# Performance work log

Measured on AMD Instinct MI355X. Metric: run time of the kernel, lower is better.

## Reference

```python
import jax, jax.numpy as jnp
import numpy as np

N = 27            # hardcoded node count in the module
D = 1024          # state_dim
E = D * 5         # MHA embed dim = 5120
H = 4             # n_heads


def setup_inputs() -> dict:
    key = jax.random.key(0)
    ks = jax.random.split(key, 6)
    s = 0.02
    return {
        "node_states": jax.random.normal(ks[0], (N, D, 5), jnp.float32),
        "hist_prev": jax.random.normal(ks[1], (N, D, 5), jnp.float32),
        "granger_w": jax.random.normal(ks[2], (1, 2 * E), jnp.float32) * s,
        "granger_b": jnp.zeros((1,), jnp.float32),
        "in_proj_w": jax.random.normal(ks[3], (3 * E, E), jnp.float32) * s,
        "in_proj_b": jnp.zeros((3 * E,), jnp.float32),
        "out_proj_w": jax.random.normal(ks[4], (E, E), jnp.float32) * s,
        "out_proj_b": jnp.zeros((E,), jnp.float32),
        "light_hertz": 500,
    }


def _mha(x, in_w, in_b, out_w, out_b):
    # x: [N, E]; torch MultiheadAttention with q=k=v=x, batch of 1
    qkv = x @ in_w.T + in_b                       # [N, 3E]
    q, k, v = jnp.split(qkv, 3, axis=-1)          # each [N, E]
    hd = E // H
    q = q.reshape(N, H, hd).transpose(1, 0, 2)    # [H, N, hd]
    k = k.reshape(N, H, hd).transpose(1, 0, 2)
    v = v.reshape(N, H, hd).transpose(1, 0, 2)
    scores = jnp.einsum('hqd,hkd->hqk', q, k) / jnp.sqrt(jnp.float32(hd))
    attn = jax.nn.softmax(scores, axis=-1)        # [H, N, N]
    o = jnp.einsum('hqk,hkd->hqd', attn, v)       # [H, N, hd]
    o = o.transpose(1, 0, 2).reshape(N, E)
    return o @ out_w.T + out_b                    # [N, E]


def reference(node_states, hist_prev, granger_w, granger_b,
              in_proj_w, in_proj_b, out_proj_w, out_proj_b, light_hertz):
    node_flat = node_states.reshape(N, E)         # [N, E]
    hist_flat = hist_prev.reshape(N, E)           # [N, E]

    # Granger pairwise test, vectorized: pred_input = [hist[j], node[i]]
    # score[i, j] = sigmoid(hist[j] . w_h + node[i] . w_n + b)
    w_h = granger_w[0, :E]
    w_n = granger_w[0, E:]
    col = node_flat @ w_n                          # [N] -> varies with i
    row = hist_flat @ w_h                          # [N] -> varies with j
    adj = jax.nn.sigmoid(col[:, None] + row[None, :] + granger_b[0])  # [N, N]
    causal_adj = adj * (1.0 - jnp.eye(N, dtype=adj.dtype))            # zero diagonal

    hertz_weight = jnp.clip(jnp.float32(light_hertz) / 1000.0, 0.1, 1.0)
    attended = _mha(node_flat, in_proj_w, in_proj_b, out_proj_w, out_proj_b)
    out = (attended * hertz_weight).reshape(N, D, 5)
    return out, causal_adj
```

## Files before the change

kernel.cpp:

```cpp
#include <hip/hip_runtime.h>

#define NROW 27
#define EDIM 5120
#define QKVDIM 15360
#define HD 1280

typedef __attribute__((ext_vector_type(8))) short bf16x8;
typedef __attribute__((ext_vector_type(4))) float f32x4;

__device__ inline short f2bf(float x) {
    unsigned u = __builtin_bit_cast(unsigned, x);
    u = (u + 0x7FFFu + ((u >> 16) & 1u)) >> 16;
    return (short)u;
}
__device__ inline float bf2f(short h) {
    unsigned u = ((unsigned)(unsigned short)h) << 16;
    return __builtin_bit_cast(float, u);
}

#define KC 64
#define LDK 72

__device__ inline void loadW8(float* wbuf, const float* wp) {
    #pragma unroll
    for (int i = 0; i < 8; ++i)
        *(float4*)&wbuf[4 * i] = ((const float4*)wp)[i];
}
__device__ inline void loadX2(float* xbuf, const float* xp, bool xok) {
    if (xok) {
        *(float4*)&xbuf[0] = ((const float4*)xp)[0];
        *(float4*)&xbuf[4] = ((const float4*)xp)[1];
    } else {
        #pragma unroll
        for (int j = 0; j < 8; ++j) xbuf[j] = 0.f;
    }
}

__global__ __launch_bounds__(256)
void gemm_bf16x2(const float* __restrict__ X, const float* __restrict__ W,
                 float* __restrict__ Cp, int K, int Ntot, int Kblk)
{
    __shared__ short Whi[128][LDK];
    __shared__ short Wlo[128][LDK];
    __shared__ short Xhi[32][LDK];
    __shared__ short Xlo[32][LDK];

    const int tid = threadIdx.x;
    const int n0 = blockIdx.x * 128;
    const int k0 = blockIdx.y * Kblk;

    const int lane = tid & 63;
    const int wv   = tid >> 6;
    const int lm   = lane & 15;
    const int q8   = (lane >> 4) * 8;

    f32x4 acc[2][2] = {};

    const int wr  = tid >> 1;
    const int wkh = (tid & 1) * 32;
    const float* wp = W + (size_t)(n0 + wr) * K + k0 + wkh;
    const int xr = tid >> 3;
    const int xk = (tid & 7) * 8;
    const bool xok = (xr < NROW);
    const float* xp = X + (size_t)(xok ? xr : 0) * K + k0 + xk;

    float wbuf[32], xbuf[8];
    loadW8(wbuf, wp);
    loadX2(xbuf, xp, xok);

    for (int kc = 0; kc < Kblk; kc += KC) {
        #pragma unroll
        for (int g = 0; g < 4; ++g) {
            bf16x8 h8, l8;
            #pragma unroll
            for (int j = 0; j < 8; ++j) {
                float f = wbuf[8 * g + j];
                short h = f2bf(f);
                h8[j] = h;
                l8[j] = f2bf(f - bf2f(h));
            }
            *(bf16x8*)&Whi[wr][wkh + 8 * g] = h8;
            *(bf16x8*)&Wlo[wr][wkh + 8 * g] = l8;
        }
        {
            bf16x8 h8, l8;
            #pragma unroll
            for (int j = 0; j < 8; ++j) {
                short h = f2bf(xbuf[j]);
                h8[j] = h;
                l8[j] = f2bf(xbuf[j] - bf2f(h));
            }
            *(bf16x8*)&Xhi[xr][xk] = h8;
            *(bf16x8*)&Xlo[xr][xk] = l8;
        }
        __syncthreads();

        if (kc + KC < Kblk) {
            wp += KC; xp += KC;
            loadW8(wbuf, wp);
            loadX2(xbuf, xp, xok);
        }

        #pragma unroll
        for (int s = 0; s < 2; ++s) {
            const int ko = 32 * s + q8;
            bf16x8 ah0 = *(const bf16x8*)&Xhi[lm][ko];
            bf16x8 ah1 = *(const bf16x8*)&Xhi[lm + 16][ko];
            bf16x8 al0 = *(const bf16x8*)&Xlo[lm][ko];
            bf16x8 al1 = *(const bf16x8*)&Xlo[lm + 16][ko];
            bf16x8 bh0 = *(const bf16x8*)&Whi[32 * wv + lm][ko];
            bf16x8 bh1 = *(const bf16x8*)&Whi[32 * wv + 16 + lm][ko];
            bf16x8 bl0 = *(const bf16x8*)&Wlo[32 * wv + lm][ko];
            bf16x8 bl1 = *(const bf16x8*)&Wlo[32 * wv + 16 + lm][ko];

            acc[0][0] = __builtin_amdgcn_mfma_f32_16x16x32_bf16(ah0, bh0, acc[0][0], 0, 0, 0);
            acc[0][0] = __builtin_amdgcn_mfma_f32_16x16x32_bf16(ah0, bl0, acc[0][0], 0, 0, 0);
            acc[0][0] = __builtin_amdgcn_mfma_f32_16x16x32_bf16(al0, bh0, acc[0][0], 0, 0, 0);

            acc[0][1] = __builtin_amdgcn_mfma_f32_16x16x32_bf16(ah0, bh1, acc[0][1], 0, 0, 0);
            acc[0][1] = __builtin_amdgcn_mfma_f32_16x16x32_bf16(ah0, bl1, acc[0][1], 0, 0, 0);
            acc[0][1] = __builtin_amdgcn_mfma_f32_16x16x32_bf16(al0, bh1, acc[0][1], 0, 0, 0);

            acc[1][0] = __builtin_amdgcn_mfma_f32_16x16x32_bf16(ah1, bh0, acc[1][0], 0, 0, 0);
            acc[1][0] = __builtin_amdgcn_mfma_f32_16x16x32_bf16(ah1, bl0, acc[1][0], 0, 0, 0);
            acc[1][0] = __builtin_amdgcn_mfma_f32_16x16x32_bf16(al1, bh0, acc[1][0], 0, 0, 0);

            acc[1][1] = __builtin_amdgcn_mfma_f32_16x16x32_bf16(ah1, bh1, acc[1][1], 0, 0, 0);
            acc[1][1] = __builtin_amdgcn_mfma_f32_16x16x32_bf16(ah1, bl1, acc[1][1], 0, 0, 0);
            acc[1][1] = __builtin_amdgcn_mfma_f32_16x16x32_bf16(al1, bh1, acc[1][1], 0, 0, 0);
        }
        __syncthreads();
    }

    const size_t base = (size_t)blockIdx.y * NROW * Ntot;
    #pragma unroll
    for (int mi = 0; mi < 2; ++mi) {
        #pragma unroll
        for (int r = 0; r < 4; ++r) {
            const int m = mi * 16 + (lane >> 4) * 4 + r;
            if (m < NROW) {
                #pragma unroll
                for (int ni = 0; ni < 2; ++ni) {
                    const int n = n0 + 32 * wv + ni * 16 + lm;
                    Cp[base + (size_t)m * Ntot + n] = acc[mi][ni][r];
                }
            }
        }
    }
}

__global__ __launch_bounds__(256)
void reduce_kernel(const float* __restrict__ Cp, const float* __restrict__ bias,
                   float* __restrict__ out, int Ntot, int nky, const int* __restrict__ hz,
                   const float* __restrict__ cr, const float* __restrict__ gb,
                   float* __restrict__ adj)
{
    if (adj && blockIdx.x == gridDim.x - 1) {
        for (int t = threadIdx.x; t < NROW * NROW; t += 256) {
            const int i = t / NROW, j = t % NROW;
            float v = 0.f;
            if (i != j) {
                float z = cr[i] + cr[NROW + j] + gb[0];
                v = 1.0f / (1.0f + expf(-z));
            }
            adj[t] = v;
        }
        return;
    }
    const int idx = blockIdx.x * 256 + threadIdx.x;
    const int total4 = NROW * Ntot / 4;
    if (idx >= total4) return;
    float4 s = ((const float4*)Cp)[idx];
    for (int k = 1; k < nky; ++k) {
        float4 p = ((const float4*)(Cp + (size_t)k * NROW * Ntot))[idx];
        s.x += p.x; s.y += p.y; s.z += p.z; s.w += p.w;
    }
    const int n = (idx * 4) % Ntot;
    float4 b = *(const float4*)(bias + n);
    s.x += b.x; s.y += b.y; s.z += b.z; s.w += b.w;
    if (hz) {
        float h = (float)hz[0] * 0.001f;
        float sc = fminf(fmaxf(h, 0.1f), 1.0f);
        s.x *= sc; s.y *= sc; s.z *= sc; s.w *= sc;
    }
    ((float4*)out)[idx] = s;
}

__global__ __launch_bounds__(256)
void colrow_kernel(const float* __restrict__ node, const float* __restrict__ hist,
                   const float* __restrict__ gw, float* __restrict__ cr)
{
    const int b = blockIdx.x;
    const float* x = (b < NROW) ? node + (size_t)b * EDIM : hist + (size_t)(b - NROW) * EDIM;
    const float* w = (b < NROW) ? gw + EDIM : gw;
    const int tid = threadIdx.x;
    float a = 0.f;
    for (int f = tid; f < EDIM / 4; f += 256) {
        float4 xv = ((const float4*)x)[f];
        float4 wv = ((const float4*)w)[f];
        a += xv.x * wv.x + xv.y * wv.y + xv.z * wv.z + xv.w * wv.w;
    }
    #pragma unroll
    for (int off = 32; off; off >>= 1) a += __shfl_down(a, off);
    __shared__ float red[4];
    if ((tid & 63) == 0) red[tid >> 6] = a;
    __syncthreads();
    if (tid == 0) cr[b] = red[0] + red[1] + red[2] + red[3];
}

__global__ __launch_bounds__(256)
void attn_kernel(const float* __restrict__ qkv, float* __restrict__ O)
{
    __shared__ float qs[HD];
    __shared__ float sc[NROW];
    __shared__ float pr[NROW];
    const int bx = blockIdx.x;
    const int h = bx & 3;
    const int i = bx >> 2;
    const int tid = threadIdx.x;

    const size_t qoff = (size_t)i * QKVDIM + (size_t)h * HD;
    for (int d = tid; d < HD; d += 256) qs[d] = qkv[qoff + d];
    __syncthreads();

    const int wid = tid >> 6, lane = tid & 63;
    for (int j = wid; j < NROW; j += 4) {
        const float* kr = qkv + (size_t)j * QKVDIM + EDIM + (size_t)h * HD;
        float a = 0.f;
        #pragma unroll
        for (int it = 0; it < 5; ++it) {
            int d4 = lane + 64 * it;
            float4 k4 = *(const float4*)(kr + 4 * d4);
            float4 q4 = *(const float4*)(qs + 4 * d4);
            a += q4.x * k4.x + q4.y * k4.y + q4.z * k4.z + q4.w * k4.w;
        }
        #pragma unroll
        for (int off = 32; off; off >>= 1) a += __shfl_down(a, off);
        if (lane == 0) sc[j] = a * 0.02795084971874737f;
    }
    __syncthreads();

    float mxv = -1e30f;
    for (int j = 0; j < NROW; ++j) mxv = fmaxf(mxv, sc[j]);
    float s = 0.f;
    for (int j = 0; j < NROW; ++j) s += expf(sc[j] - mxv);
    if (tid < NROW) pr[tid] = expf(sc[tid] - mxv) / s;
    __syncthreads();

    for (int d4 = tid; d4 < HD / 4; d4 += 256) {
        float4 o = make_float4(0.f, 0.f, 0.f, 0.f);
        for (int j = 0; j < NROW; ++j) {
            const float4 v4 = *(const float4*)(qkv + (size_t)j * QKVDIM + 2 * EDIM + (size_t)h * HD + 4 * d4);
            const float p = pr[j];
            o.x = fmaf(p, v4.x, o.x);
            o.y = fmaf(p, v4.y, o.y);
            o.z = fmaf(p, v4.z, o.z);
            o.w = fmaf(p, v4.w, o.w);
        }
        *(float4*)(O + (size_t)i * EDIM + (size_t)h * HD + 4 * d4) = o;
    }
}

extern "C" void kernel_launch(void* const* d_in, const int* in_sizes, int n_in,
                              void* d_out, int out_size, void* d_ws, size_t ws_size,
                              hipStream_t stream)
{
    const float* node = (const float*)d_in[0];
    const float* hist = (const float*)d_in[1];
    const float* gw   = (const float*)d_in[2];
    const float* gb   = (const float*)d_in[3];
    const float* inw  = (const float*)d_in[4];
    const float* inb  = (const float*)d_in[5];
    const float* outw = (const float*)d_in[6];
    const float* outb = (const float*)d_in[7];
    const int*   hz   = (const int*)d_in[8];

    float* out = (float*)d_out;

    float* Cp1  = (float*)d_ws;
    float* qkvf = Cp1 + (size_t)8 * NROW * QKVDIM;
    float* Obuf = qkvf + (size_t)NROW * QKVDIM;
    float* Cp2  = Obuf + (size_t)NROW * EDIM;
    float* cr   = Cp2 + (size_t)16 * NROW * EDIM;

    colrow_kernel<<<54, 256, 0, stream>>>(node, hist, gw, cr);

    gemm_bf16x2<<<dim3(120, 8), 256, 0, stream>>>(node, inw, Cp1, EDIM, QKVDIM, EDIM / 8);
    reduce_kernel<<<NROW * QKVDIM / 4 / 256, 256, 0, stream>>>(
        Cp1, inb, qkvf, QKVDIM, 8, nullptr, nullptr, nullptr, nullptr);

    attn_kernel<<<108, 256, 0, stream>>>(qkvf, Obuf);

    gemm_bf16x2<<<dim3(40, 16), 256, 0, stream>>>(Obuf, outw, Cp2, EDIM, EDIM, EDIM / 16);
    reduce_kernel<<<NROW * EDIM / 4 / 256 + 1, 256, 0, stream>>>(
        Cp2, outb, out, EDIM, 16, hz, cr, gb, out + (size_t)NROW * EDIM);
}
```

Measured before the change: 542.2 us.

## Load weight MFMA fragments directly into registers, double-buffer X tile in LDS

```diff
diff --git a/kernel.cpp b/kernel.cpp
--- a/kernel.cpp
+++ b/kernel.cpp
@@ -21,11 +21,6 @@
 #define KC 64
 #define LDK 72
 
-__device__ inline void loadW8(float* wbuf, const float* wp) {
-    #pragma unroll
-    for (int i = 0; i < 8; ++i)
-        *(float4*)&wbuf[4 * i] = ((const float4*)wp)[i];
-}
 __device__ inline void loadX2(float* xbuf, const float* xp, bool xok) {
     if (xok) {
         *(float4*)&xbuf[0] = ((const float4*)xp)[0];
@@ -36,14 +31,22 @@
     }
 }
 
-__global__ __launch_bounds__(256)
-void gemm_bf16x2(const float* __restrict__ X, const float* __restrict__ W,
-                 float* __restrict__ Cp, int K, int Ntot, int Kblk)
-{
-    __shared__ short Whi[128][LDK];
-    __shared__ short Wlo[128][LDK];
-    __shared__ short Xhi[32][LDK];
-    __shared__ short Xlo[32][LDK];
+__device__ inline void loadWfrag(float4* wreg, const float* wp0, const float* wp1) {
+    #pragma unroll
+    for (int s = 0; s < 2; ++s) {
+        wreg[s * 2 + 0] = *(const float4*)(wp0 + 32 * s);
+        wreg[s * 2 + 1] = *(const float4*)(wp0 + 32 * s + 4);
+        wreg[4 + s * 2 + 0] = *(const float4*)(wp1 + 32 * s);
+        wreg[4 + s * 2 + 1] = *(const float4*)(wp1 + 32 * s + 4);
+    }
+}
+
+__global__ __launch_bounds__(256, 3)
+void gemm_regw(const float* __restrict__ X, const float* __restrict__ W,
+               float* __restrict__ Cp, int K, int Ntot, int Kblk)
+{
+    __shared__ __align__(16) short Xhi[2][32][LDK];
+    __shared__ __align__(16) short Xlo[2][32][LDK];
 
     const int tid = threadIdx.x;
     const int n0 = blockIdx.x * 128;
@@ -56,32 +59,23 @@
 
     f32x4 acc[2][2] = {};
 
-    const int wr  = tid >> 1;
-    const int wkh = (tid & 1) * 32;
-    const float* wp = W + (size_t)(n0 + wr) * K + k0 + wkh;
     const int xr = tid >> 3;
     const int xk = (tid & 7) * 8;
     const bool xok = (xr < NROW);
     const float* xp = X + (size_t)(xok ? xr : 0) * K + k0 + xk;
 
-    float wbuf[32], xbuf[8];
-    loadW8(wbuf, wp);
+    const float* wp0 = W + (size_t)(n0 + 32 * wv + lm) * K + k0 + q8;
+    const float* wp1 = wp0 + (size_t)16 * K;
+
+    float  xbuf[8];
+    float4 wreg[8];
+
     loadX2(xbuf, xp, xok);
-
-    for (int kc = 0; kc < Kblk; kc += KC) {
-        #pragma unroll
-        for (int g = 0; g < 4; ++g) {
-            bf16x8 h8, l8;
-            #pragma unroll
-            for (int j = 0; j < 8; ++j) {
-                float f = wbuf[8 * g + j];
-                short h = f2bf(f);
-                h8[j] = h;
-                l8[j] = f2bf(f - bf2f(h));
-            }
-            *(bf16x8*)&Whi[wr][wkh + 8 * g] = h8;
-            *(bf16x8*)&Wlo[wr][wkh + 8 * g] = l8;
-        }
+    loadWfrag(wreg, wp0, wp1);
+
+    const int nc = Kblk / KC;
+    int p = 0;
+    for (int c = 0; c < nc; ++c) {
         {
             bf16x8 h8, l8;
             #pragma unroll
@@ -90,46 +84,65 @@
                 h8[j] = h;
                 l8[j] = f2bf(xbuf[j] - bf2f(h));
             }
-            *(bf16x8*)&Xhi[xr][xk] = h8;
-            *(bf16x8*)&Xlo[xr][xk] = l8;
-        }
+            *(bf16x8*)&Xhi[p][xr][xk] = h8;
+            *(bf16x8*)&Xlo[p][xr][xk] = l8;
+        }
+
+        bf16x8 whi[2][2], wlo[2][2];
+        #pragma unroll
+        for (int g = 0; g < 2; ++g) {
+            #pragma unroll
+            for (int s = 0; s < 2; ++s) {
+                const float4 a = wreg[g * 4 + s * 2 + 0];
+                const float4 b = wreg[g * 4 + s * 2 + 1];
+                const float f[8] = {a.x, a.y, a.z, a.w, b.x, b.y, b.z, b.w};
+                bf16x8 h8, l8;
+                #pragma unroll
+                for (int j = 0; j < 8; ++j) {
+                    short h = f2bf(f[j]);
+                    h8[j] = h;
+                    l8[j] = f2bf(f[j] - bf2f(h));
+                }
+                whi[s][g] = h8;
+                wlo[s][g] = l8;
+            }
+        }
+
+        if (c + 1 < nc) {
+            xp  += KC;
+            wp0 += KC;
+            wp1 += KC;
+            loadX2(xbuf, xp, xok);
+            loadWfrag(wreg, wp0, wp1);
+        }
+
         __syncthreads();
-
-        if (kc + KC < Kblk) {
-            wp += KC; xp += KC;
-            loadW8(wbuf, wp);
-            loadX2(xbuf, xp, xok);
-        }
 
         #pragma unroll
         for (int s = 0; s < 2; ++s) {
             const int ko = 32 * s + q8;
-            bf16x8 ah0 = *(const bf16x8*)&Xhi[lm][ko];
-            bf16x8 ah1 = *(const bf16x8*)&Xhi[lm + 16][ko];
-            bf16x8 al0 = *(const bf16x8*)&Xlo[lm][ko];
-            bf16x8 al1 = *(const bf16x8*)&Xlo[lm + 16][ko];
-            bf16x8 bh0 = *(const bf16x8*)&Whi[32 * wv + lm][ko];
-            bf16x8 bh1 = *(const bf16x8*)&Whi[32 * wv + 16 + lm][ko];
-            bf16x8 bl0 = *(const bf16x8*)&Wlo[32 * wv + lm][ko];
-            bf16x8 bl1 = *(const bf16x8*)&Wlo[32 * wv + 16 + lm][ko];
-
-            acc[0][0] = __builtin_amdgcn_mfma_f32_16x16x32_bf16(ah0, bh0, acc[0][0], 0, 0, 0);
-            acc[0][0] = __builtin_amdgcn_mfma_f32_16x16x32_bf16(ah0, bl0, acc[0][0], 0, 0, 0);
-            acc[0][0] = __builtin_amdgcn_mfma_f32_16x16x32_bf16(al0, bh0, acc[0][0], 0, 0, 0);
-
-            acc[0][1] = __builtin_amdgcn_mfma_f32_16x16x32_bf16(ah0, bh1, acc[0][1], 0, 0, 0);
-            acc[0][1] = __builtin_amdgcn_mfma_f32_16x16x32_bf16(ah0, bl1, acc[0][1], 0, 0, 0);
-            acc[0][1] = __builtin_amdgcn_mfma_f32_16x16x32_bf16(al0, bh1, acc[0][1], 0, 0, 0);
-
-            acc[1][0] = __builtin_amdgcn_mfma_f32_16x16x32_bf16(ah1, bh0, acc[1][0], 0, 0, 0);
-            acc[1][0] = __builtin_amdgcn_mfma_f32_16x16x32_bf16(ah1, bl0, acc[1][0], 0, 0, 0);
-            acc[1][0] = __builtin_amdgcn_mfma_f32_16x16x32_bf16(al1, bh0, acc[1][0], 0, 0, 0);
-
-            acc[1][1] = __builtin_amdgcn_mfma_f32_16x16x32_bf16(ah1, bh1, acc[1][1], 0, 0, 0);
-            acc[1][1] = __builtin_amdgcn_mfma_f32_16x16x32_bf16(ah1, bl1, acc[1][1], 0, 0, 0);
-            acc[1][1] = __builtin_amdgcn_mfma_f32_16x16x32_bf16(al1, bh1, acc[1][1], 0, 0, 0);
-        }
-        __syncthreads();
+            bf16x8 ah0 = *(const bf16x8*)&Xhi[p][lm][ko];
+            bf16x8 ah1 = *(const bf16x8*)&Xhi[p][lm + 16][ko];
+            bf16x8 al0 = *(const bf16x8*)&Xlo[p][lm][ko];
+            bf16x8 al1 = *(const bf16x8*)&Xlo[p][lm + 16][ko];
+
+            acc[0][0] = __builtin_amdgcn_mfma_f32_16x16x32_bf16(ah0, whi[s][0], acc[0][0], 0, 0, 0);
+            acc[0][0] = __builtin_amdgcn_mfma_f32_16x16x32_bf16(ah0, wlo[s][0], acc[0][0], 0, 0, 0);
+            acc[0][0] = __builtin_amdgcn_mfma_f32_16x16x32_bf16(al0, whi[s][0], acc[0][0], 0, 0, 0);
+
+            acc[0][1] = __builtin_amdgcn_mfma_f32_16x16x32_bf16(ah0, whi[s][1], acc[0][1], 0, 0, 0);
+            acc[0][1] = __builtin_amdgcn_mfma_f32_16x16x32_bf16(ah0, wlo[s][1], acc[0][1], 0, 0, 0);
+            acc[0][1] = __builtin_amdgcn_mfma_f32_16x16x32_bf16(al0, whi[s][1], acc[0][1], 0, 0, 0);
+
+            acc[1][0] = __builtin_amdgcn_mfma_f32_16x16x32_bf16(ah1, whi[s][0], acc[1][0], 0, 0, 0);
+            acc[1][0] = __builtin_amdgcn_mfma_f32_16x16x32_bf16(ah1, wlo[s][0], acc[1][0], 0, 0, 0);
+            acc[1][0] = __builtin_amdgcn_mfma_f32_16x16x32_bf16(al1, whi[s][0], acc[1][0], 0, 0, 0);
+
+            acc[1][1] = __builtin_amdgcn_mfma_f32_16x16x32_bf16(ah1, whi[s][1], acc[1][1], 0, 0, 0);
+            acc[1][1] = __builtin_amdgcn_mfma_f32_16x16x32_bf16(ah1, wlo[s][1], acc[1][1], 0, 0, 0);
+            acc[1][1] = __builtin_amdgcn_mfma_f32_16x16x32_bf16(al1, whi[s][1], acc[1][1], 0, 0, 0);
+        }
+        p ^= 1;
     }
 
     const size_t base = (size_t)blockIdx.y * NROW * Ntot;
@@ -285,13 +298,13 @@
 
     colrow_kernel<<<54, 256, 0, stream>>>(node, hist, gw, cr);
 
-    gemm_bf16x2<<<dim3(120, 8), 256, 0, stream>>>(node, inw, Cp1, EDIM, QKVDIM, EDIM / 8);
+    gemm_regw<<<dim3(120, 8), 256, 0, stream>>>(node, inw, Cp1, EDIM, QKVDIM, EDIM / 8);
     reduce_kernel<<<NROW * QKVDIM / 4 / 256, 256, 0, stream>>>(
         Cp1, inb, qkvf, QKVDIM, 8, nullptr, nullptr, nullptr, nullptr);
 
     attn_kernel<<<108, 256, 0, stream>>>(qkvf, Obuf);
 
-    gemm_bf16x2<<<dim3(40, 16), 256, 0, stream>>>(Obuf, outw, Cp2, EDIM, EDIM, EDIM / 16);
+    gemm_regw<<<dim3(40, 16), 256, 0, stream>>>(Obuf, outw, Cp2, EDIM, EDIM, EDIM / 16);
     reduce_kernel<<<NROW * EDIM / 4 / 256 + 1, 256, 0, stream>>>(
         Cp2, outb, out, EDIM, 16, hz, cr, gb, out + (size_t)NROW * EDIM);
 }
```

Measured after the change: 534.5 us. About the same (-1.4%).
